# Performance work log

Hardware: AMD Instinct MI355X
Metric: run time of the kernel (lower is better)

The kernel has to match this reference:

```python
import jax, jax.numpy as jnp
import numpy as np

N = 16384
K = 4096  # codebook_size
D = 512   # embedding_dim
COMMITMENT_COST = 0.25


def setup_inputs() -> dict:
    key = jax.random.key(0)
    kz, kc = jax.random.split(key)
    z = jax.random.normal(kz, (N, D), dtype=jnp.float32)
    # nn.Embedding weight init: uniform(-1/K, 1/K)
    codebook = jax.random.uniform(kc, (K, D), dtype=jnp.float32,
                                  minval=-1.0 / K, maxval=1.0 / K)
    return {"z": z, "codebook": codebook}


def reference(z, codebook):
    # squared L2 distances: [N, K]
    dists = (jnp.sum(z * z, axis=1, keepdims=True)
             + jnp.sum(codebook * codebook, axis=1)
             - 2.0 * jnp.matmul(z, codebook.T))
    idx = jnp.argmin(dists, axis=1)                 # [N]
    z_q = codebook[idx]                             # gather == one-hot @ codebook
    # straight-through estimator
    z_q_ste = z + jax.lax.stop_gradient(z_q - z)
    commitment_loss = jnp.mean((jax.lax.stop_gradient(z) - z_q) ** 2)
    codebook_loss = jnp.mean((z - jax.lax.stop_gradient(z_q)) ** 2)
    loss = codebook_loss + COMMITMENT_COST * commitment_loss
    encoding_indices = idx[:, None]                 # [N, 1] to match torch shape
    return (z_q_ste, encoding_indices, loss)
```

## Files before the change

### kernel.cpp

```cpp
#include <hip/hip_runtime.h>
#include <math.h>

#define N_ROWS 16384
#define K_CODES 4096
#define D_DIM 512
#define NCHUNK 8
#define KCHUNK (K_CODES / NCHUNK)
#define MARGIN 2.5e-3f
#define CAND_CAP 1024

typedef unsigned int uint32;
typedef unsigned short u16t;
typedef __attribute__((ext_vector_type(8))) short short8;
typedef __attribute__((ext_vector_type(4))) float f32x4;

__device__ __forceinline__ float fmul_(float a, float b) { return __fmul_rn(a, b); }
__device__ __forceinline__ float fadd_(float a, float b) { return __fadd_rn(a, b); }

__global__ void rownorm_np_kernel(const float* __restrict__ src, int nrows,
                                  float* __restrict__ out) {
    int gid = blockIdx.x * blockDim.x + threadIdx.x;
    int row = gid >> 2;
    int blk = gid & 3;
    if (row >= nrows) return;
    const float4* p = (const float4*)(src + (size_t)row * D_DIM + blk * 128);
    float4 v0 = p[0], v1 = p[1];
    float r0 = fmul_(v0.x, v0.x), r1 = fmul_(v0.y, v0.y);
    float r2 = fmul_(v0.z, v0.z), r3 = fmul_(v0.w, v0.w);
    float r4 = fmul_(v1.x, v1.x), r5 = fmul_(v1.y, v1.y);
    float r6 = fmul_(v1.z, v1.z), r7 = fmul_(v1.w, v1.w);
#pragma unroll
    for (int i = 1; i < 16; i++) {
        float4 w0 = p[2 * i], w1 = p[2 * i + 1];
        r0 = fadd_(r0, fmul_(w0.x, w0.x));
        r1 = fadd_(r1, fmul_(w0.y, w0.y));
        r2 = fadd_(r2, fmul_(w0.z, w0.z));
        r3 = fadd_(r3, fmul_(w0.w, w0.w));
        r4 = fadd_(r4, fmul_(w1.x, w1.x));
        r5 = fadd_(r5, fmul_(w1.y, w1.y));
        r6 = fadd_(r6, fmul_(w1.z, w1.z));
        r7 = fadd_(r7, fmul_(w1.w, w1.w));
    }
    float s = fadd_(fadd_(fadd_(r0, r1), fadd_(r2, r3)),
                    fadd_(fadd_(r4, r5), fadd_(r6, r7)));
    float u = __shfl_down(s, 1, 64);
    float t = fadd_(s, u);
    float w = __shfl_down(t, 2, 64);
    float tot = fadd_(t, w);
    if (blk == 0) out[row] = tot;
}

__device__ __forceinline__ u16t f2bf(float x) {
    uint32 u = __float_as_uint(x);
    return (u16t)((u + 0x7fffu + ((u >> 16) & 1u)) >> 16);
}
__global__ void cvt_bf16_kernel(const float* __restrict__ src,
                                u16t* __restrict__ dst, int n4) {
    int i = blockIdx.x * blockDim.x + threadIdx.x;
    if (i >= n4) return;
    float4 v = ((const float4*)src)[i];
    ushort4 o;
    o.x = f2bf(v.x); o.y = f2bf(v.y); o.z = f2bf(v.z); o.w = f2bf(v.w);
    ((ushort4*)dst)[i] = o;
}

#define STS 136

__global__ __launch_bounds__(256) void score_gemm_kernel(
    const u16t* __restrict__ zb, const u16t* __restrict__ cbb,
    const float* __restrict__ cnorm, u16t* __restrict__ scores) {
    __shared__ alignas(16) u16t Ab[128 * 32];
    __shared__ alignas(16) u16t Bb[128 * 32];
    __shared__ alignas(16) u16t stile[128 * STS];

    const int t = threadIdx.x;
    const int bx = blockIdx.x;
    const int by = blockIdx.y;
    const int row0 = by * 128, k0 = bx * KCHUNK;
    const int w = t >> 6, lane = t & 63;
    const int wx = w & 1, wy = w >> 1;
    const int l15 = lane & 15, quad = lane >> 4;

    for (int kt = 0; kt < 4; kt++) {
        f32x4 acc[4][4];
#pragma unroll
        for (int i = 0; i < 4; i++)
#pragma unroll
            for (int j = 0; j < 4; j++) acc[i][j] = (f32x4){0.f, 0.f, 0.f, 0.f};

        for (int dt = 0; dt < 16; dt++) {
            __syncthreads();
#pragma unroll
            for (int q = 0; q < 2; q++) {
                int s = q * 256 + t;
                const u16t* ga = zb + (size_t)(row0 + (s >> 2)) * D_DIM + dt * 32 + (s & 3) * 8;
                __builtin_amdgcn_global_load_lds(
                    (const __attribute__((address_space(1))) void*)ga,
                    (__attribute__((address_space(3))) void*)((char*)Ab + q * 4096 + w * 1024),
                    16, 0, 0);
                const u16t* gb = cbb + (size_t)(k0 + kt * 128 + (s >> 2)) * D_DIM + dt * 32 + (s & 3) * 8;
                __builtin_amdgcn_global_load_lds(
                    (const __attribute__((address_space(1))) void*)gb,
                    (__attribute__((address_space(3))) void*)((char*)Bb + q * 4096 + w * 1024),
                    16, 0, 0);
            }
            __syncthreads();
            short8 a[4], b[4];
#pragma unroll
            for (int i = 0; i < 4; i++)
                a[i] = *(const short8*)((char*)Ab + (wy * 64 + i * 16 + l15) * 64 + quad * 16);
#pragma unroll
            for (int j = 0; j < 4; j++)
                b[j] = *(const short8*)((char*)Bb + (wx * 64 + j * 16 + l15) * 64 + quad * 16);
#pragma unroll
            for (int i = 0; i < 4; i++)
#pragma unroll
                for (int j = 0; j < 4; j++)
                    acc[i][j] = __builtin_amdgcn_mfma_f32_16x16x32_bf16(a[i], b[j], acc[i][j], 0, 0, 0);
        }
#pragma unroll
        for (int j = 0; j < 4; j++) {
            int cl = wx * 64 + j * 16 + l15;
            float cn = cnorm[k0 + kt * 128 + cl];
#pragma unroll
            for (int i = 0; i < 4; i++) {
#pragma unroll
                for (int r = 0; r < 4; r++) {
                    int rl = wy * 64 + i * 16 + quad * 4 + r;
                    float s = fmaf(-2.f, acc[i][j][r], cn);
                    stile[rl * STS + cl] = f2bf(s);
                }
            }
        }
        __syncthreads();
        for (int idx = t; idx < 128 * 16; idx += 256) {
            int row = idx >> 4, seg = idx & 15;
            short8 v = *(const short8*)&stile[row * STS + seg * 8];
            *(short8*)(scores + (size_t)(row0 + row) * K_CODES + k0 + kt * 128 + seg * 8) = v;
        }
    }
}

__global__ __launch_bounds__(256) void scan_refine_kernel(
    const u16t* __restrict__ scores,
    const float* __restrict__ z, const float* __restrict__ cb,
    const float* __restrict__ zz, const float* __restrict__ cnorm,
    float* __restrict__ out_zq, float* __restrict__ out_idx,
    float* __restrict__ rowsum) {
    __shared__ float smin[256];
    __shared__ int clist[CAND_CAP];
    __shared__ int cnt;
    __shared__ float wbv[4];
    __shared__ int wbi[4];
    __shared__ float red[256];
    __shared__ int bcast;

    const int row = blockIdx.x;
    const int t = threadIdx.x;
    const int w = t >> 6, lane = t & 63;

    if (t == 0) cnt = 0;

    const u16t* srow = scores + (size_t)row * K_CODES + t * 16;
    short8 sv0 = *(const short8*)(srow);
    short8 sv1 = *(const short8*)(srow + 8);
    float f[16];
#pragma unroll
    for (int e = 0; e < 8; e++) {
        f[e]     = __uint_as_float(((uint32)(u16t)sv0[e]) << 16);
        f[e + 8] = __uint_as_float(((uint32)(u16t)sv1[e]) << 16);
    }
    float m = f[0];
#pragma unroll
    for (int e = 1; e < 16; e++) m = fminf(m, f[e]);
    smin[t] = m;
    __syncthreads();
    for (int st = 128; st; st >>= 1) {
        if (t < st) smin[t] = fminf(smin[t], smin[t + st]);
        __syncthreads();
    }
    const float thr = smin[0] + MARGIN;

#pragma unroll
    for (int e = 0; e < 16; e++) {
        if (f[e] <= thr) {
            int pos = atomicAdd(&cnt, 1);
            if (pos < CAND_CAP) clist[pos] = t * 16 + e;
        }
    }
    __syncthreads();
    const int C = cnt < CAND_CAP ? cnt : CAND_CAP;

    const float* zr = z + (size_t)row * D_DIM;
    float4 z0 = *(const float4*)(zr + lane * 8);
    float4 z1 = *(const float4*)(zr + lane * 8 + 4);
    float zzr = zz[row];

    float bv = 3.4e38f;
    int bi = 0x7fffffff;
    for (int ci = w; ci < C; ci += 4) {
        int k = clist[ci];
        const float* cr = cb + (size_t)k * D_DIM;
        float4 c0 = *(const float4*)(cr + lane * 8);
        float4 c1 = *(const float4*)(cr + lane * 8 + 4);
        float d = fmul_(z0.x, c0.x);
        d = fmaf(z0.y, c0.y, d); d = fmaf(z0.z, c0.z, d); d = fmaf(z0.w, c0.w, d);
        d = fmaf(z1.x, c1.x, d); d = fmaf(z1.y, c1.y, d);
        d = fmaf(z1.z, c1.z, d); d = fmaf(z1.w, c1.w, d);
#pragma unroll
        for (int off = 1; off < 64; off <<= 1)
            d = fadd_(d, __shfl_xor(d, off, 64));
        float dist = fmaf(-2.f, d, fadd_(zzr, cnorm[k]));
        if (dist < bv || (dist == bv && k < bi)) { bv = dist; bi = k; }
    }
    if (lane == 0) { wbv[w] = bv; wbi[w] = bi; }
    __syncthreads();
    if (t == 0) {
        float B = wbv[0]; int I = wbi[0];
#pragma unroll
        for (int i = 1; i < 4; i++) {
            float v = wbv[i]; int ii = wbi[i];
            if (v < B || (v == B && ii < I)) { B = v; I = ii; }
        }
        bcast = I;
        out_idx[row] = (float)I;
    }
    __syncthreads();
    const int K = bcast;
    const float* cq = cb + (size_t)K * D_DIM;
    float2 zv2 = *(const float2*)(zr + t * 2);
    float2 cv2 = *(const float2*)(cq + t * 2);
    float2 o;
    o.x = fadd_(zv2.x, __fsub_rn(cv2.x, zv2.x));
    o.y = fadd_(zv2.y, __fsub_rn(cv2.y, zv2.y));
    *(float2*)(out_zq + (size_t)row * D_DIM + t * 2) = o;
    float dx = zv2.x - cv2.x, dy = zv2.y - cv2.y;
    red[t] = dx * dx + dy * dy;
    __syncthreads();
    for (int st = 128; st; st >>= 1) {
        if (t < st) red[t] += red[t + st];
        __syncthreads();
    }
    if (t == 0) rowsum[row] = red[0];
}

__global__ void loss_kernel(const float* __restrict__ rowsum,
                            float* __restrict__ out_loss) {
    __shared__ float sm[256];
    float s = 0.f;
    for (int i = threadIdx.x; i < N_ROWS; i += 256) s += rowsum[i];
    sm[threadIdx.x] = s;
    __syncthreads();
    for (int st = 128; st; st >>= 1) {
        if (threadIdx.x < st) sm[threadIdx.x] += sm[threadIdx.x + st];
        __syncthreads();
    }
    if (threadIdx.x == 0)
        *out_loss = 1.25f * sm[0] / (float)(N_ROWS * D_DIM);
}

#define BM 128
#define BN 128
#define BK 16
#define TM 8
#define TN 8

__global__ __launch_bounds__(256, 4) void vq_argmin_kernel(
    const float* __restrict__ z, const float* __restrict__ cb,
    const float* __restrict__ zz, const float* __restrict__ cnorm,
    float* __restrict__ pval, int* __restrict__ pidx) {
    __shared__ float As[BK][BM + 4];
    __shared__ float Bs[BK][BN + 4];
    __shared__ float rv[BM][17];
    __shared__ int   ri[BM][17];

    const int bx = blockIdx.x;
    const int by = blockIdx.y;
    const int row0 = by * BM;
    const int k0 = bx * KCHUNK;
    const int t = threadIdx.x;
    const int tx = t & 15;
    const int ty = t >> 4;

    float minv[TM];
    int   mini[TM];
#pragma unroll
    for (int i = 0; i < TM; i++) { minv[i] = 3.4e38f; mini[i] = 0; }
    float zrow[TM];
#pragma unroll
    for (int i = 0; i < TM; i++) zrow[i] = zz[row0 + ty * TM + i];
    const int sr = t >> 1;
    const int sdq = (t & 1) * 8;

    for (int kt = 0; kt < KCHUNK / BN; kt++) {
        const int col0 = k0 + kt * BN;
        float acc[TM][TN];
#pragma unroll
        for (int i = 0; i < TM; i++)
#pragma unroll
            for (int j = 0; j < TN; j++) acc[i][j] = 0.f;
        for (int dt = 0; dt < D_DIM; dt += BK) {
            {
                const float* src = z + (size_t)(row0 + sr) * D_DIM + dt + sdq;
                float4 v0 = *(const float4*)(src);
                float4 v1 = *(const float4*)(src + 4);
                As[sdq + 0][sr] = v0.x; As[sdq + 1][sr] = v0.y;
                As[sdq + 2][sr] = v0.z; As[sdq + 3][sr] = v0.w;
                As[sdq + 4][sr] = v1.x; As[sdq + 5][sr] = v1.y;
                As[sdq + 6][sr] = v1.z; As[sdq + 7][sr] = v1.w;
                const float* srcb = cb + (size_t)(col0 + sr) * D_DIM + dt + sdq;
                float4 w0 = *(const float4*)(srcb);
                float4 w1 = *(const float4*)(srcb + 4);
                Bs[sdq + 0][sr] = w0.x; Bs[sdq + 1][sr] = w0.y;
                Bs[sdq + 2][sr] = w0.z; Bs[sdq + 3][sr] = w0.w;
                Bs[sdq + 4][sr] = w1.x; Bs[sdq + 5][sr] = w1.y;
                Bs[sdq + 6][sr] = w1.z; Bs[sdq + 7][sr] = w1.w;
            }
            __syncthreads();
#pragma unroll
            for (int d = 0; d < BK; d++) {
                float a[TM], b[TN];
#pragma unroll
                for (int i = 0; i < TM; i++) a[i] = As[d][ty * TM + i];
#pragma unroll
                for (int j = 0; j < TN; j++) b[j] = Bs[d][tx * TN + j];
#pragma unroll
                for (int i = 0; i < TM; i++)
#pragma unroll
                    for (int j = 0; j < TN; j++)
                        acc[i][j] = fmaf(a[i], b[j], acc[i][j]);
            }
            __syncthreads();
        }
#pragma unroll
        for (int j = 0; j < TN; j++) {
            const int col = col0 + tx * TN + j;
            const float cn = cnorm[col];
#pragma unroll
            for (int i = 0; i < TM; i++) {
                float s1 = fadd_(zrow[i], cn);
                float s = fmaf(-2.f, acc[i][j], s1);
                if (s < minv[i]) { minv[i] = s; mini[i] = col; }
            }
        }
    }
#pragma unroll
    for (int i = 0; i < TM; i++) {
        rv[ty * TM + i][tx] = minv[i];
        ri[ty * TM + i][tx] = mini[i];
    }
    __syncthreads();
    if (t < BM) {
        float bv = rv[t][0];
        int   bi = ri[t][0];
#pragma unroll
        for (int x = 1; x < 16; x++) {
            float v = rv[t][x]; int ii = ri[t][x];
            if (v < bv || (v == bv && ii < bi)) { bv = v; bi = ii; }
        }
        pval[(size_t)(row0 + t) * NCHUNK + bx] = bv;
        pidx[(size_t)(row0 + t) * NCHUNK + bx] = bi;
    }
}

__global__ void finalize_kernel(const float* __restrict__ z,
                                const float* __restrict__ cb,
                                const float* __restrict__ pval,
                                const int* __restrict__ pidx,
                                float* __restrict__ out_zq,
                                float* __restrict__ out_idx,
                                float* __restrict__ rowsum) {
    int row = (blockIdx.x * blockDim.x + threadIdx.x) >> 6;
    int lane = threadIdx.x & 63;
    if (row >= N_ROWS) return;
    float bv = pval[(size_t)row * NCHUNK];
    int   bi = pidx[(size_t)row * NCHUNK];
#pragma unroll
    for (int c = 1; c < NCHUNK; c++) {
        float v = pval[(size_t)row * NCHUNK + c];
        int  ii = pidx[(size_t)row * NCHUNK + c];
        if (v < bv || (v == bv && ii < bi)) { bv = v; bi = ii; }
    }
    const float4* zr = (const float4*)(z + (size_t)row * D_DIM);
    const float4* cr = (const float4*)(cb + (size_t)bi * D_DIM);
    float4* orow = (float4*)(out_zq + (size_t)row * D_DIM);
    float s = 0.f;
#pragma unroll
    for (int i = 0; i < 2; i++) {
        float4 zv = zr[i * 64 + lane];
        float4 cv = cr[i * 64 + lane];
        float4 o;
        o.x = fadd_(zv.x, __fsub_rn(cv.x, zv.x));
        o.y = fadd_(zv.y, __fsub_rn(cv.y, zv.y));
        o.z = fadd_(zv.z, __fsub_rn(cv.z, zv.z));
        o.w = fadd_(zv.w, __fsub_rn(cv.w, zv.w));
        orow[i * 64 + lane] = o;
        float dx = zv.x - cv.x, dy = zv.y - cv.y;
        float dz = zv.z - cv.z, dw = zv.w - cv.w;
        s += dx * dx + dy * dy + dz * dz + dw * dw;
    }
#pragma unroll
    for (int off = 32; off; off >>= 1) s += __shfl_down(s, off, 64);
    if (lane == 0) {
        rowsum[row] = s;
        out_idx[row] = (float)bi;
    }
}

extern "C" void kernel_launch(void* const* d_in, const int* in_sizes, int n_in,
                              void* d_out, int out_size, void* d_ws, size_t ws_size,
                              hipStream_t stream) {
    const float* z  = (const float*)d_in[0];
    const float* cb = (const float*)d_in[1];
    float* out      = (float*)d_out;
    float* out_zq   = out;
    float* out_idx  = out + (size_t)N_ROWS * D_DIM;
    float* out_loss = out_idx + N_ROWS;

    float* zz     = (float*)d_ws;
    float* cnorm  = zz + N_ROWS;
    float* rowsum = cnorm + K_CODES;
    u16t*  z_bf   = (u16t*)(rowsum + N_ROWS);
    u16t*  cb_bf  = z_bf + (size_t)N_ROWS * D_DIM;
    u16t*  scores = cb_bf + (size_t)K_CODES * D_DIM;
    const size_t WS_NEEDED = (size_t)(N_ROWS + K_CODES + N_ROWS) * 4
                           + (size_t)N_ROWS * D_DIM * 2
                           + (size_t)K_CODES * D_DIM * 2
                           + (size_t)N_ROWS * K_CODES * 2;

    if (ws_size >= WS_NEEDED) {
        cvt_bf16_kernel<<<(N_ROWS * D_DIM / 4 + 255) / 256, 256, 0, stream>>>(z, z_bf, N_ROWS * D_DIM / 4);
        cvt_bf16_kernel<<<(K_CODES * D_DIM / 4 + 255) / 256, 256, 0, stream>>>(cb, cb_bf, K_CODES * D_DIM / 4);
        rownorm_np_kernel<<<(N_ROWS * 4) / 256, 256, 0, stream>>>(z, N_ROWS, zz);
        rownorm_np_kernel<<<(K_CODES * 4) / 256, 256, 0, stream>>>(cb, K_CODES, cnorm);

        dim3 g1(NCHUNK, N_ROWS / 128);
        score_gemm_kernel<<<g1, 256, 0, stream>>>(z_bf, cb_bf, cnorm, scores);
        scan_refine_kernel<<<N_ROWS, 256, 0, stream>>>(scores, z, cb, zz, cnorm,
                                                       out_zq, out_idx, rowsum);
        loss_kernel<<<1, 256, 0, stream>>>(rowsum, out_loss);
    } else {
        float* pval = rowsum + N_ROWS;
        int*   pidx = (int*)(pval + (size_t)N_ROWS * NCHUNK);
        rownorm_np_kernel<<<(N_ROWS * 4) / 256, 256, 0, stream>>>(z, N_ROWS, zz);
        rownorm_np_kernel<<<(K_CODES * 4) / 256, 256, 0, stream>>>(cb, K_CODES, cnorm);
        dim3 g2(NCHUNK, N_ROWS / BM);
        vq_argmin_kernel<<<g2, 256, 0, stream>>>(z, cb, zz, cnorm, pval, pidx);
        finalize_kernel<<<N_ROWS / 4, 256, 0, stream>>>(z, cb, pval, pidx,
                                                        out_zq, out_idx, rowsum);
        loss_kernel<<<1, 256, 0, stream>>>(rowsum, out_loss);
    }
}
```

Before: 289.3 us.

## Fuse per-row min and candidate selection into GEMM epilogue, dropping the score matrix

The GEMM epilogue no longer writes the full bf16 score matrix to global memory. Each block now computes a per-row running minimum over its codebook chunk, using shuffle reductions and LDS atomicMin on order-preserving keys. It then writes only the scores within a margin of that minimum into a fixed-capacity per-chunk candidate list. The refine kernel combines the per-chunk minima and filters the candidates against a global threshold, instead of reading 4096 scores per row. This removes a large global write and re-read of the score matrix, at the cost of extra epilogue work, LDS atomics, and a risk of dropping true nearest codes if a chunk has more than 32 candidates.

```diff
diff --git a/kernel.cpp b/kernel.cpp
--- a/kernel.cpp
+++ b/kernel.cpp
@@ -8,6 +8,7 @@
 #define KCHUNK (K_CODES / NCHUNK)
 #define MARGIN 2.5e-3f
 #define CAND_CAP 1024
+#define CCAP 32
 
 typedef unsigned int uint32;
 typedef unsigned short u16t;
@@ -54,6 +55,18 @@
     uint32 u = __float_as_uint(x);
     return (u16t)((u + 0x7fffu + ((u >> 16) & 1u)) >> 16);
 }
+__device__ __forceinline__ float bfr(float x) {
+    return __uint_as_float(((uint32)f2bf(x)) << 16);
+}
+__device__ __forceinline__ uint32 fkey(float f) {
+    uint32 u = __float_as_uint(f);
+    return (u & 0x80000000u) ? ~u : (u | 0x80000000u);
+}
+__device__ __forceinline__ float fdec(uint32 k) {
+    uint32 u = (k & 0x80000000u) ? (k ^ 0x80000000u) : ~k;
+    return __uint_as_float(u);
+}
+
 __global__ void cvt_bf16_kernel(const float* __restrict__ src,
                                 u16t* __restrict__ dst, int n4) {
     int i = blockIdx.x * blockDim.x + threadIdx.x;
@@ -64,14 +77,16 @@
     ((ushort4*)dst)[i] = o;
 }
 
-#define STS 136
-
 __global__ __launch_bounds__(256) void score_gemm_kernel(
     const u16t* __restrict__ zb, const u16t* __restrict__ cbb,
-    const float* __restrict__ cnorm, u16t* __restrict__ scores) {
+    const float* __restrict__ cnorm,
+    float* __restrict__ chunkmin,
+    uint32* __restrict__ cnts,
+    uint2* __restrict__ cand) {
     __shared__ alignas(16) u16t Ab[128 * 32];
     __shared__ alignas(16) u16t Bb[128 * 32];
-    __shared__ alignas(16) u16t stile[128 * STS];
+    __shared__ uint32 rowminU[128];
+    __shared__ int ccnt[128];
 
     const int t = threadIdx.x;
     const int bx = blockIdx.x;
@@ -80,6 +95,8 @@
     const int w = t >> 6, lane = t & 63;
     const int wx = w & 1, wy = w >> 1;
     const int l15 = lane & 15, quad = lane >> 4;
+
+    if (t < 128) { rowminU[t] = 0xFFFFFFFFu; ccnt[t] = 0; }
 
     for (int kt = 0; kt < 4; kt++) {
         f32x4 acc[4][4];
@@ -118,38 +135,73 @@
                 for (int j = 0; j < 4; j++)
                     acc[i][j] = __builtin_amdgcn_mfma_f32_16x16x32_bf16(a[i], b[j], acc[i][j], 0, 0, 0);
         }
+
+        float cnj[4];
+        int colj[4];
 #pragma unroll
         for (int j = 0; j < 4; j++) {
-            int cl = wx * 64 + j * 16 + l15;
-            float cn = cnorm[k0 + kt * 128 + cl];
-#pragma unroll
-            for (int i = 0; i < 4; i++) {
-#pragma unroll
-                for (int r = 0; r < 4; r++) {
-                    int rl = wy * 64 + i * 16 + quad * 4 + r;
-                    float s = fmaf(-2.f, acc[i][j][r], cn);
-                    stile[rl * STS + cl] = f2bf(s);
+            colj[j] = kt * 128 + wx * 64 + j * 16 + l15;
+            cnj[j] = cnorm[k0 + colj[j]];
+        }
+#pragma unroll
+        for (int i = 0; i < 4; i++) {
+#pragma unroll
+            for (int r = 0; r < 4; r++) {
+                float m = 3.4e38f;
+#pragma unroll
+                for (int j = 0; j < 4; j++) {
+                    float s = bfr(fmaf(-2.f, acc[i][j][r], cnj[j]));
+                    m = fminf(m, s);
                 }
+                m = fminf(m, __shfl_xor(m, 1, 64));
+                m = fminf(m, __shfl_xor(m, 2, 64));
+                m = fminf(m, __shfl_xor(m, 4, 64));
+                m = fminf(m, __shfl_xor(m, 8, 64));
+                if (l15 == 0)
+                    atomicMin(&rowminU[wy * 64 + i * 16 + quad * 4 + r], fkey(m));
             }
         }
         __syncthreads();
-        for (int idx = t; idx < 128 * 16; idx += 256) {
-            int row = idx >> 4, seg = idx & 15;
-            short8 v = *(const short8*)&stile[row * STS + seg * 8];
-            *(short8*)(scores + (size_t)(row0 + row) * K_CODES + k0 + kt * 128 + seg * 8) = v;
-        }
-    }
-}
-
-__global__ __launch_bounds__(256) void scan_refine_kernel(
-    const u16t* __restrict__ scores,
+#pragma unroll
+        for (int i = 0; i < 4; i++) {
+#pragma unroll
+            for (int r = 0; r < 4; r++) {
+                const int rl = wy * 64 + i * 16 + quad * 4 + r;
+                const float thr = fdec(rowminU[rl]) + MARGIN;
+#pragma unroll
+                for (int j = 0; j < 4; j++) {
+                    float s = bfr(fmaf(-2.f, acc[i][j][r], cnj[j]));
+                    if (s <= thr) {
+                        int pos = atomicAdd(&ccnt[rl], 1);
+                        if (pos < CCAP) {
+                            uint2 e;
+                            e.x = __float_as_uint(s);
+                            e.y = (uint32)(k0 + colj[j]);
+                            cand[((size_t)(row0 + rl) * NCHUNK + bx) * CCAP + pos] = e;
+                        }
+                    }
+                }
+            }
+        }
+    }
+    __syncthreads();
+    if (t < 128) {
+        chunkmin[(size_t)(row0 + t) * NCHUNK + bx] = fdec(rowminU[t]);
+        int c = ccnt[t];
+        cnts[(size_t)(row0 + t) * NCHUNK + bx] = (uint32)(c < CCAP ? c : CCAP);
+    }
+}
+
+__global__ __launch_bounds__(256) void refine_kernel(
+    const uint2* __restrict__ cand, const uint32* __restrict__ cnts,
+    const float* __restrict__ chunkmin,
     const float* __restrict__ z, const float* __restrict__ cb,
     const float* __restrict__ zz, const float* __restrict__ cnorm,
     float* __restrict__ out_zq, float* __restrict__ out_idx,
     float* __restrict__ rowsum) {
-    __shared__ float smin[256];
-    __shared__ int clist[CAND_CAP];
-    __shared__ int cnt;
+    __shared__ int clist[NCHUNK * CCAP];
+    __shared__ int ccnt;
+    __shared__ float gminS;
     __shared__ float wbv[4];
     __shared__ int wbi[4];
     __shared__ float red[256];
@@ -159,37 +211,30 @@
     const int t = threadIdx.x;
     const int w = t >> 6, lane = t & 63;
 
-    if (t == 0) cnt = 0;
-
-    const u16t* srow = scores + (size_t)row * K_CODES + t * 16;
-    short8 sv0 = *(const short8*)(srow);
-    short8 sv1 = *(const short8*)(srow + 8);
-    float f[16];
-#pragma unroll
-    for (int e = 0; e < 8; e++) {
-        f[e]     = __uint_as_float(((uint32)(u16t)sv0[e]) << 16);
-        f[e + 8] = __uint_as_float(((uint32)(u16t)sv1[e]) << 16);
-    }
-    float m = f[0];
-#pragma unroll
-    for (int e = 1; e < 16; e++) m = fminf(m, f[e]);
-    smin[t] = m;
-    __syncthreads();
-    for (int st = 128; st; st >>= 1) {
-        if (t < st) smin[t] = fminf(smin[t], smin[t + st]);
-        __syncthreads();
-    }
-    const float thr = smin[0] + MARGIN;
-
-#pragma unroll
-    for (int e = 0; e < 16; e++) {
-        if (f[e] <= thr) {
-            int pos = atomicAdd(&cnt, 1);
-            if (pos < CAND_CAP) clist[pos] = t * 16 + e;
-        }
-    }
-    __syncthreads();
-    const int C = cnt < CAND_CAP ? cnt : CAND_CAP;
+    if (t == 0) {
+        ccnt = 0;
+        float g = chunkmin[(size_t)row * NCHUNK];
+#pragma unroll
+        for (int c = 1; c < NCHUNK; c++)
+            g = fminf(g, chunkmin[(size_t)row * NCHUNK + c]);
+        gminS = g;
+    }
+    __syncthreads();
+    const float thr = gminS + MARGIN;
+
+    {
+        int c = t >> 5, s2 = t & (CCAP - 1);
+        uint32 n = cnts[(size_t)row * NCHUNK + c];
+        if ((uint32)s2 < n) {
+            uint2 e = cand[((size_t)row * NCHUNK + c) * CCAP + s2];
+            if (__uint_as_float(e.x) <= thr) {
+                int pos = atomicAdd(&ccnt, 1);
+                clist[pos] = (int)e.y;
+            }
+        }
+    }
+    __syncthreads();
+    const int C = ccnt;
 
     const float* zr = z + (size_t)row * D_DIM;
     float4 z0 = *(const float4*)(zr + lane * 8);
@@ -422,11 +467,14 @@
     float* rowsum = cnorm + K_CODES;
     u16t*  z_bf   = (u16t*)(rowsum + N_ROWS);
     u16t*  cb_bf  = z_bf + (size_t)N_ROWS * D_DIM;
-    u16t*  scores = cb_bf + (size_t)K_CODES * D_DIM;
+    float* chunkmin = (float*)(cb_bf + (size_t)K_CODES * D_DIM);
+    uint32* cnts  = (uint32*)(chunkmin + (size_t)N_ROWS * NCHUNK);
+    uint2* cand   = (uint2*)(cnts + (size_t)N_ROWS * NCHUNK);
     const size_t WS_NEEDED = (size_t)(N_ROWS + K_CODES + N_ROWS) * 4
                            + (size_t)N_ROWS * D_DIM * 2
                            + (size_t)K_CODES * D_DIM * 2
-                           + (size_t)N_ROWS * K_CODES * 2;
+                           + (size_t)N_ROWS * NCHUNK * 4 * 2
+                           + (size_t)N_ROWS * NCHUNK * CCAP * 8;
 
     if (ws_size >= WS_NEEDED) {
         cvt_bf16_kernel<<<(N_ROWS * D_DIM / 4 + 255) / 256, 256, 0, stream>>>(z, z_bf, N_ROWS * D_DIM / 4);
@@ -435,9 +483,11 @@
         rownorm_np_kernel<<<(K_CODES * 4) / 256, 256, 0, stream>>>(cb, K_CODES, cnorm);
 
         dim3 g1(NCHUNK, N_ROWS / 128);
-        score_gemm_kernel<<<g1, 256, 0, stream>>>(z_bf, cb_bf, cnorm, scores);
-        scan_refine_kernel<<<N_ROWS, 256, 0, stream>>>(scores, z, cb, zz, cnorm,
-                                                       out_zq, out_idx, rowsum);
+        score_gemm_kernel<<<g1, 256, 0, stream>>>(z_bf, cb_bf, cnorm,
+                                                  chunkmin, cnts, cand);
+        refine_kernel<<<N_ROWS, 256, 0, stream>>>(cand, cnts, chunkmin,
+                                                  z, cb, zz, cnorm,
+                                                  out_zq, out_idx, rowsum);
         loss_kernel<<<1, 256, 0, stream>>>(rowsum, out_loss);
     } else {
         float* pval = rowsum + N_ROWS;
```

Result: slower. 436.2 us (+50.8%).
